# Kernel optimization log

Measured on AMD Instinct MI355X. Metric: run time of the kernel, lower is better.

## Reference

```python
import jax, jax.numpy as jnp
import numpy as np

TOP_K_PCT = 0.1
MAX_SHARP_TOKENS = 10
SMOOTHING = 0.1


def setup_inputs() -> dict:
    key = jax.random.key(0)
    logits = jax.random.normal(key, (2, 8, 2048, 2048), dtype=jnp.float32)
    return {"logits": logits, "dim": 3}


def reference(logits, dim):
    # Move the softmax axis to the end so lax.top_k / row-scatter apply.
    x = jnp.moveaxis(logits, dim, -1)
    N = x.shape[-1]
    k = min(MAX_SHARP_TOKENS, max(1, int(N * TOP_K_PCT)))

    vals, idx = jax.lax.top_k(x, k)            # [..., k], sorted descending
    topk_soft = jax.nn.softmax(vals, axis=-1)  # softmax over just the top-k values

    flat = x.reshape(-1, N)                    # [R, N]
    fidx = idx.reshape(-1, k)                  # [R, k]
    rows = jnp.arange(flat.shape[0])[:, None]

    # boolean mask of top-k positions
    mask = jnp.zeros(flat.shape, dtype=bool).at[rows, fidx].set(True)

    # softmax over the remaining (non-top-k) logits; top-k filled with dtype min
    neg_inf = jnp.finfo(flat.dtype).min
    remaining = jnp.where(mask, neg_inf, flat)
    rem_soft = jax.nn.softmax(remaining, axis=-1)
    rem_soft = jnp.where(mask, jnp.zeros((), flat.dtype), rem_soft)

    # scatter top-k softmax back, then blend
    final = jnp.zeros_like(flat).at[rows, fidx].set(topk_soft.reshape(-1, k))
    out = final * (1.0 - SMOOTHING) + rem_soft * SMOOTHING

    return jnp.moveaxis(out.reshape(x.shape), -1, dim)
```

## Files before the change

### kernel.cpp

```cpp
#include <hip/hip_runtime.h>
#include <math.h>

#define ROW_N 2048
#define KSEL 10
#define WCAP 64

typedef float f32x4 __attribute__((ext_vector_type(4)));
typedef unsigned long long u64;

__global__ __launch_bounds__(256, 6) void topk_softmax_kernel(
    const float* __restrict__ in, float* __restrict__ out)
{
    const int lane = threadIdx.x & 63;
    const int wave = threadIdx.x >> 6;
    const size_t base = ((size_t)blockIdx.x * 4 + wave) * ROW_N;

    __shared__ u64 s_cand[4][WCAP];

    const f32x4* p4 = reinterpret_cast<const f32x4*>(in + base);
    f32x4 V[8];
    #pragma unroll
    for (int j = 0; j < 8; ++j) V[j] = p4[j * 64 + lane];

    float vm = -INFINITY;
    #pragma unroll
    for (int j = 0; j < 8; ++j)
        #pragma unroll
        for (int c = 0; c < 4; ++c) vm = fmaxf(vm, V[j][c]);
    #pragma unroll
    for (int off = 32; off > 0; off >>= 1) vm = fmaxf(vm, __shfl_xor(vm, off));

    const int low0 = 2047 - lane * 4;
    float Tf = 2.2f;
    float dlt = 0.35f;
    int C = 0;
    #pragma unroll 1
    for (int t = 0; t < 8; ++t) {
        C = 0;
        #pragma unroll
        for (int j = 0; j < 8; ++j)
            #pragma unroll
            for (int c = 0; c < 4; ++c) {
                bool cond = V[j][c] > Tf;
                u64 m = __ballot(cond);
                if (cond) {
                    uint32_t u  = __float_as_uint(V[j][c]);
                    uint32_t ov = u ^ ((uint32_t)((int32_t)u >> 31) | 0x80000000u);
                    int pos = C + (int)__builtin_amdgcn_mbcnt_hi(
                                      (unsigned)(m >> 32),
                                      __builtin_amdgcn_mbcnt_lo((unsigned)m, 0u));
                    if (pos < WCAP)
                        s_cand[wave][pos] =
                            ((u64)ov << 16) | (unsigned)(low0 - (j * 256 + c));
                }
                C += __popcll(m);
            }
        if (C >= KSEL && C <= WCAP) break;
        Tf += (C < KSEL) ? -dlt : dlt;
        dlt *= 2.f;
    }
    if (C > WCAP) C = WCAP;

    u64 k0 = (lane < C) ? s_cand[wave][lane] : 0ULL;
    const uint32_t ov0 = (uint32_t)(k0 >> 16);

    const float K  = 1.4426950408889634f;
    const float c0 = -vm * K;
    float tot = 0.f;
    #pragma unroll
    for (int j = 0; j < 8; ++j) {
        f32x4 e;
        #pragma unroll
        for (int c = 0; c < 4; ++c) { e[c] = exp2f(fmaf(V[j][c], K, c0)); tot += e[c]; }
        V[j] = e;
    }

    uint32_t kov = 0;
    #pragma unroll
    for (int b = 31; b >= 0; --b) {
        uint32_t trial = kov | (1u << b);
        if (__popcll(__ballot(ov0 >= trial)) >= KSEL) kov = trial;
    }
    u64 kmin = ((u64)kov) << 16;
    int W = __popcll(__ballot(ov0 >= kov));
    if (W != KSEL) {
        kmin = 0ULL;
        #pragma unroll 1
        for (int b = 47; b >= 0; --b) {
            u64 trial = kmin | (1ULL << b);
            if (__popcll(__ballot(k0 >= trial)) >= KSEL) kmin = trial;
        }
    }
    const bool win = (k0 >= kmin) && (k0 != 0ULL);

    uint32_t bits = ov0 ^ ((ov0 & 0x80000000u) ? 0x80000000u : 0xFFFFFFFFu);
    float val = __uint_as_float(bits);
    float ee  = win ? exp2f(fmaf(val, K, c0)) : 0.f;

    float ssum = ee;
    #pragma unroll
    for (int off = 32; off > 0; off >>= 1) {
        tot  += __shfl_xor(tot, off);
        ssum += __shfl_xor(ssum, off);
    }

    const float aa = 0.9f / ssum;
    const float bb = 0.1f / (tot - ssum);

    f32x4* o4 = reinterpret_cast<f32x4*>(out + base);
    #pragma unroll
    for (int j = 0; j < 8; ++j) {
        f32x4 o;
        #pragma unroll
        for (int c = 0; c < 4; ++c) o[c] = V[j][c] * bb;
        __builtin_nontemporal_store(o, o4 + j * 64 + lane);
    }
    asm volatile("s_waitcnt vmcnt(0)" ::: "memory");
    if (win) out[base + 2047 - (int)(k0 & 0xFFFFull)] = ee * aa;
}

extern "C" void kernel_launch(void* const* d_in, const int* in_sizes, int n_in,
                              void* d_out, int out_size, void* d_ws, size_t ws_size,
                              hipStream_t stream) {
    const float* logits = (const float*)d_in[0];
    float* out = (float*)d_out;
    const int rows = out_size / ROW_N;
    topk_softmax_kernel<<<dim3(rows / 4), dim3(256), 0, stream>>>(logits, out);
}
```

Before: 532.1 us.

## Select top-k threshold from per-lane top-2 radix search and fuse scatter into store

Each lane now tracks its two largest values, and a wave-wide 32-bit radix search over those 64x2 candidates finds the 10th-largest threshold directly. This replaces the iterative guessed-threshold candidate compaction loop through shared memory. Exponentials are taken without max subtraction to form the total, which is rescaled afterwards. Top-k positions are written inline during the vectorized store, so the second scattered store and its waitcnt are gone, at the cost of recomputing exp per element in the output loop. A fallback path handles lanes holding more than two winners or ties. Launch bounds drop the occupancy hint of 6, and the unshifted exp2 could overflow for large logits.

```diff
diff --git a/kernel.cpp b/kernel.cpp
--- a/kernel.cpp
+++ b/kernel.cpp
@@ -8,7 +8,7 @@
 typedef float f32x4 __attribute__((ext_vector_type(4)));
 typedef unsigned long long u64;
 
-__global__ __launch_bounds__(256, 6) void topk_softmax_kernel(
+__global__ __launch_bounds__(256) void topk_softmax_kernel(
     const float* __restrict__ in, float* __restrict__ out)
 {
     const int lane = threadIdx.x & 63;
@@ -22,26 +22,80 @@
     #pragma unroll
     for (int j = 0; j < 8; ++j) V[j] = p4[j * 64 + lane];
 
-    float vm = -INFINITY;
+    const float K = 1.4426950408889634f;
+    float m1 = -INFINITY, m2 = -INFINITY, tot0 = 0.f;
     #pragma unroll
     for (int j = 0; j < 8; ++j)
         #pragma unroll
-        for (int c = 0; c < 4; ++c) vm = fmaxf(vm, V[j][c]);
+        for (int c = 0; c < 4; ++c) {
+            float x = V[j][c];
+            m2 = fmaxf(fminf(x, m1), m2);
+            m1 = fmaxf(x, m1);
+            tot0 += exp2f(x * K);
+        }
+
+    float vm = m1;
     #pragma unroll
-    for (int off = 32; off > 0; off >>= 1) vm = fmaxf(vm, __shfl_xor(vm, off));
+    for (int off = 32; off > 0; off >>= 1) {
+        vm = fmaxf(vm, __shfl_xor(vm, off));
+        tot0 += __shfl_xor(tot0, off);
+    }
 
-    const int low0 = 2047 - lane * 4;
-    float Tf = 2.2f;
-    float dlt = 0.35f;
-    int C = 0;
-    #pragma unroll 1
-    for (int t = 0; t < 8; ++t) {
-        C = 0;
+    uint32_t u1 = __float_as_uint(m1);
+    uint32_t u2 = __float_as_uint(m2);
+    const uint32_t o1 = u1 ^ ((uint32_t)((int32_t)u1 >> 31) | 0x80000000u);
+    const uint32_t o2 = u2 ^ ((uint32_t)((int32_t)u2 >> 31) | 0x80000000u);
+    uint32_t kov = 0;
+    #pragma unroll
+    for (int b = 31; b >= 0; --b) {
+        uint32_t t = kov | (1u << b);
+        int cnt = __popcll(__ballot(o1 >= t)) + __popcll(__ballot(o2 >= t));
+        if (cnt >= KSEL) kov = t;
+    }
+    const uint32_t kb = kov ^ ((kov & 0x80000000u) ? 0x80000000u : 0xFFFFFFFFu);
+    const float kf = __uint_as_float(kb);
+
+    int wc = 0;
+    #pragma unroll
+    for (int j = 0; j < 8; ++j)
+        #pragma unroll
+        for (int c = 0; c < 4; ++c) wc += (V[j][c] >= kf) ? 1 : 0;
+    #pragma unroll
+    for (int off = 32; off > 0; off >>= 1) wc += __shfl_xor(wc, off);
+
+    const float c0v = -vm * K;
+    const float tot = tot0 * exp2f(c0v);
+
+    f32x4* o4 = reinterpret_cast<f32x4*>(out + base);
+
+    if (wc == KSEL) {
+        float e1 = (m1 >= kf) ? exp2f(fmaf(m1, K, c0v)) : 0.f;
+        float e2 = (m2 >= kf) ? exp2f(fmaf(m2, K, c0v)) : 0.f;
+        float ssum = e1 + e2;
+        #pragma unroll
+        for (int off = 32; off > 0; off >>= 1) ssum += __shfl_xor(ssum, off);
+
+        const float aa = 0.9f / ssum;
+        const float bb = 0.1f / (tot - ssum);
+        #pragma unroll
+        for (int j = 0; j < 8; ++j) {
+            f32x4 o;
+            #pragma unroll
+            for (int c = 0; c < 4; ++c) {
+                float x = V[j][c];
+                float e = exp2f(fmaf(x, K, c0v));
+                o[c] = e * ((x >= kf) ? aa : bb);
+            }
+            __builtin_nontemporal_store(o, o4 + j * 64 + lane);
+        }
+    } else {
+        const int low0 = 2047 - lane * 4;
+        int C = 0;
         #pragma unroll
         for (int j = 0; j < 8; ++j)
             #pragma unroll
             for (int c = 0; c < 4; ++c) {
-                bool cond = V[j][c] > Tf;
+                bool cond = V[j][c] >= kf;
                 u64 m = __ballot(cond);
                 if (cond) {
                     uint32_t u  = __float_as_uint(V[j][c]);
@@ -55,68 +109,42 @@
                 }
                 C += __popcll(m);
             }
-        if (C >= KSEL && C <= WCAP) break;
-        Tf += (C < KSEL) ? -dlt : dlt;
-        dlt *= 2.f;
-    }
-    if (C > WCAP) C = WCAP;
+        if (C > WCAP) C = WCAP;
 
-    u64 k0 = (lane < C) ? s_cand[wave][lane] : 0ULL;
-    const uint32_t ov0 = (uint32_t)(k0 >> 16);
-
-    const float K  = 1.4426950408889634f;
-    const float c0 = -vm * K;
-    float tot = 0.f;
-    #pragma unroll
-    for (int j = 0; j < 8; ++j) {
-        f32x4 e;
-        #pragma unroll
-        for (int c = 0; c < 4; ++c) { e[c] = exp2f(fmaf(V[j][c], K, c0)); tot += e[c]; }
-        V[j] = e;
-    }
-
-    uint32_t kov = 0;
-    #pragma unroll
-    for (int b = 31; b >= 0; --b) {
-        uint32_t trial = kov | (1u << b);
-        if (__popcll(__ballot(ov0 >= trial)) >= KSEL) kov = trial;
-    }
-    u64 kmin = ((u64)kov) << 16;
-    int W = __popcll(__ballot(ov0 >= kov));
-    if (W != KSEL) {
-        kmin = 0ULL;
+        u64 k0 = (lane < C) ? s_cand[wave][lane] : 0ULL;
+        u64 kmin = 0ULL;
         #pragma unroll 1
         for (int b = 47; b >= 0; --b) {
             u64 trial = kmin | (1ULL << b);
             if (__popcll(__ballot(k0 >= trial)) >= KSEL) kmin = trial;
         }
+
+        uint32_t ovk  = (uint32_t)(k0 >> 16);
+        uint32_t bits = ovk ^ ((ovk & 0x80000000u) ? 0x80000000u : 0xFFFFFFFFu);
+        float val = __uint_as_float(bits);
+        bool win  = (k0 >= kmin) && (k0 != 0ULL);
+        float ee  = win ? exp2f(fmaf(val, K, c0v)) : 0.f;
+        float ssum = ee;
+        #pragma unroll
+        for (int off = 32; off > 0; off >>= 1) ssum += __shfl_xor(ssum, off);
+
+        const float aa = 0.9f / ssum;
+        const float bb = 0.1f / (tot - ssum);
+        #pragma unroll
+        for (int j = 0; j < 8; ++j) {
+            f32x4 o;
+            #pragma unroll
+            for (int c = 0; c < 4; ++c) {
+                float x = V[j][c];
+                uint32_t u  = __float_as_uint(x);
+                uint32_t ov = u ^ ((uint32_t)((int32_t)u >> 31) | 0x80000000u);
+                u64 key = ((u64)ov << 16) | (unsigned)(low0 - (j * 256 + c));
+                float e = exp2f(fmaf(x, K, c0v));
+                o[c] = e * ((key >= kmin) ? aa : bb);
+            }
+            __builtin_nontemporal_store(o, o4 + j * 64 + lane);
+        }
     }
-    const bool win = (k0 >= kmin) && (k0 != 0ULL);
-
-    uint32_t bits = ov0 ^ ((ov0 & 0x80000000u) ? 0x80000000u : 0xFFFFFFFFu);
-    float val = __uint_as_float(bits);
-    float ee  = win ? exp2f(fmaf(val, K, c0)) : 0.f;
-
-    float ssum = ee;
-    #pragma unroll
-    for (int off = 32; off > 0; off >>= 1) {
-        tot  += __shfl_xor(tot, off);
-        ssum += __shfl_xor(ssum, off);
-    }
-
-    const float aa = 0.9f / ssum;
-    const float bb = 0.1f / (tot - ssum);
-
-    f32x4* o4 = reinterpret_cast<f32x4*>(out + base);
-    #pragma unroll
-    for (int j = 0; j < 8; ++j) {
-        f32x4 o;
-        #pragma unroll
-        for (int c = 0; c < 4; ++c) o[c] = V[j][c] * bb;
-        __builtin_nontemporal_store(o, o4 + j * 64 + lane);
-    }
-    asm volatile("s_waitcnt vmcnt(0)" ::: "memory");
-    if (win) out[base + 2047 - (int)(k0 & 0xFFFFull)] = ee * aa;
 }
 
 extern "C" void kernel_launch(void* const* d_in, const int* in_sizes, int n_in,
```

After: 449.7 us. -15.5%, faster.
